# Performance work log

Hardware: AMD Instinct MI355X
Metric: run time of the kernel (lower is better)

The kernel has to match this reference:

```python
import jax, jax.numpy as jnp
import numpy as np

N, C, V, T = 256, 256, 25, 20
K = 3            # kernel_size
PAD = 1          # padding
O = 256          # out_channels
C4 = C // 4
EPS = 1e-5


def _bn(x, p, axes_shape):
    # p: (4, dim) = gamma, beta, running_mean, running_var (eval-mode BN)
    g, b, m, v = (p[i].reshape(axes_shape) for i in range(4))
    return (x - m) * (g / jnp.sqrt(v + EPS)) + b


def setup_inputs() -> dict:
    key = jax.random.key(0)
    ks = jax.random.split(key, 12)
    rn = lambda k, s, sc=0.05: jax.random.normal(k, s, jnp.float32) * sc
    bn = lambda k, d: jnp.stack([
        1.0 + 0.1 * jax.random.normal(jax.random.fold_in(k, 0), (d,), jnp.float32),  # gamma
        0.1 * jax.random.normal(jax.random.fold_in(k, 1), (d,), jnp.float32),        # beta
        0.1 * jax.random.normal(jax.random.fold_in(k, 2), (d,), jnp.float32),        # mean
        0.5 + jax.random.uniform(jax.random.fold_in(k, 3), (d,), jnp.float32),       # var
    ])
    return {
        "x": jax.random.normal(ks[0], (N, C, V, T), jnp.float32),
        "Wg1": rn(ks[1], (2 * T, T), 0.2),      # Linear T -> 2T (no bias)
        "Wg2": rn(ks[2], (K, 2 * T), 0.2),      # Linear 2T -> K (no bias)
        "Wl1": rn(ks[3], (C4, C, K)),           # Conv1d C -> C/4, kernel K
        "Wl2": rn(ks[4], (C, C4)),              # Conv1d C/4 -> C, kernel 1
        "Wc2": rn(ks[5], (O, C)),               # 1x1 Conv2d C -> O (no bias)
        "bng": bn(ks[6], 2 * T),
        "bnl": bn(ks[7], C4),
        "bn1p": bn(ks[8], C),
        "bn2p": bn(ks[9], O),
    }


def reference(x, Wg1, Wg2, Wl1, Wl2, Wc2, bng, bnl, bn1p, bn2p):
    n, c, v, t = x.shape
    new_x = jnp.transpose(x, (0, 1, 3, 2))            # (N, C, T, V)
    pooled = new_x.mean(axis=-1)                       # (N, C, T)  adaptive_avg_pool over V

    # --- G branch: per-(n,c) dynamic temporal kernel ---
    h = pooled.reshape(n * c, t) @ Wg1.T               # (NC, 2T)
    h = jax.nn.relu(_bn(h, bng, (1, 2 * t)))
    kern = jax.nn.softmax(h @ Wg2.T, axis=-1)          # (NC, K)
    kern = kern.reshape(n, c, K)

    # --- L branch: local temporal excitation ---
    l = jax.lax.conv_general_dilated(
        pooled, Wl1, window_strides=(1,), padding=[(K // 2, K // 2)],
        dimension_numbers=("NCH", "OIH", "NCH"))      # (N, C4, T)
    l = jax.nn.relu(_bn(l, bnl, (1, C4, 1)))
    l = jax.nn.sigmoid(jnp.einsum("oc,nct->not", Wl2, l))  # (N, C, T)
    new_x = new_x + l[..., None]                       # (N, C, T, V)

    # --- dynamic depthwise temporal conv (groups = N*C) ---
    padded = jnp.pad(new_x, ((0, 0), (0, 0), (PAD, PAD), (0, 0)))
    out = sum(kern[:, :, k, None, None] * padded[:, :, k:k + t, :] for k in range(K))

    out = jnp.transpose(out, (0, 1, 3, 2))             # (N, C, V, T)
    out = jax.nn.relu(_bn(out, bn1p, (1, c, 1, 1)))    # bn1 + relu; dropout in eval = identity
    out = jnp.einsum("oc,ncvt->novt", Wc2, out)        # 1x1 conv
    out = jax.nn.relu(_bn(out, bn2p, (1, O, 1, 1)))    # bn2 + relu
    return out
```

## Files before the change

### kernel.cpp

```cpp
#include <hip/hip_runtime.h>
#include <hip/hip_bf16.h>
#include <math.h>

#define N_ 256
#define C_ 256
#define V_ 25
#define T_ 20
#define C4_ 64
#define O_ 256
#define VT_ 500
#define EPS_ 1e-5f

typedef unsigned short ushort_t;
typedef unsigned short us4 __attribute__((ext_vector_type(4)));
typedef short short8 __attribute__((ext_vector_type(8)));
typedef float f32x4 __attribute__((ext_vector_type(4)));

__device__ __forceinline__ float bf2f(ushort_t u) {
    unsigned int v = ((unsigned int)u) << 16;
    return __builtin_bit_cast(float, v);
}
__device__ __forceinline__ ushort_t f2bf(float f) {
    unsigned int u = __builtin_bit_cast(unsigned int, f);
    unsigned int r = u + 0x7fffu + ((u >> 16) & 1u);
    return (ushort_t)(r >> 16);
}

__device__ __forceinline__ void bar_lds() {
    __builtin_amdgcn_sched_barrier(0);
    asm volatile("s_waitcnt lgkmcnt(0)" ::: "memory");
    __builtin_amdgcn_s_barrier();
    __builtin_amdgcn_sched_barrier(0);
}

__global__ __launch_bounds__(256) void k_pool(const float* __restrict__ x,
                                              float* __restrict__ pooled,
                                              const float* __restrict__ Wc2,
                                              ushort_t* __restrict__ wbf) {
    int tid = threadIdx.x;
    if (blockIdx.x >= 8192) {
        int i = (blockIdx.x - 8192) * 256 + tid;
        f32x4 v = ((const f32x4*)Wc2)[i];
        us4 o; o.x = f2bf(v.x); o.y = f2bf(v.y); o.z = f2bf(v.z); o.w = f2bf(v.w);
        ((us4*)wbf)[i] = o;
        return;
    }
    __shared__ float xs[8][504];
    const f32x4* src = (const f32x4*)(x + (size_t)blockIdx.x * 8 * VT_);
    for (int i = tid; i < 1000; i += 256) {
        int r = i / 125, cidx = (i % 125) * 4;
        *(f32x4*)&xs[r][cidx] = src[i];
    }
    __syncthreads();
    if (tid < 160) {
        int r = tid / 20, t = tid % 20;
        float s = 0.f;
#pragma unroll
        for (int v = 0; v < V_; ++v) s += xs[r][v * T_ + t];
        pooled[blockIdx.x * 160 + tid] = s * 0.04f;
    }
}

__global__ __launch_bounds__(256) void k_gl(const float* __restrict__ pooled,
                                            const float* __restrict__ Wg1,
                                            const float* __restrict__ Wg2,
                                            const float* __restrict__ Wl1,
                                            const float* __restrict__ Wl2,
                                            const float* __restrict__ bng,
                                            const float* __restrict__ bnl,
                                            float* __restrict__ kern,
                                            float* __restrict__ l2out) {
    __shared__ float pp[C_][22];
    __shared__ float wg1[800];
    __shared__ float wg2[120];
    __shared__ float sg[40], bg[40];
    __shared__ float ls[C4_][20];
    __shared__ float sl[C4_], bl[C4_];
    int tid = threadIdx.x;
    int n = blockIdx.x;

    for (int i = tid; i < 800; i += 256) wg1[i] = Wg1[i];
    if (tid < 120) wg2[tid] = Wg2[tid];
    if (tid < 40) {
        float g = bng[tid], b = bng[40 + tid];
        float m = bng[80 + tid], v = bng[120 + tid];
        float s = g * rsqrtf(v + EPS_);
        sg[tid] = s; bg[tid] = b - m * s;
    }
    if (tid < C4_) {
        float g = bnl[tid], b = bnl[64 + tid];
        float m = bnl[128 + tid], v = bnl[192 + tid];
        float s = g * rsqrtf(v + EPS_);
        sl[tid] = s; bl[tid] = b - m * s;
    }
    {
        const f32x4* pn = (const f32x4*)(pooled + n * (C_ * T_));
#pragma unroll
        for (int q = 0; q < 5; ++q) {
            int id = q * 256 + tid;
            int c = id / 5, qq = id % 5;
            f32x4 v = pn[id];
            pp[c][qq * 4 + 1] = v.x; pp[c][qq * 4 + 2] = v.y;
            pp[c][qq * 4 + 3] = v.z; pp[c][qq * 4 + 4] = v.w;
        }
        pp[tid][0] = 0.f; pp[tid][21] = 0.f;
    }
    __syncthreads();

    {
        int c = tid;
        float p[20];
#pragma unroll
        for (int t = 0; t < 20; ++t) p[t] = pp[c][t + 1];
        float l0 = 0.f, l1 = 0.f, l2 = 0.f;
#pragma unroll 4
        for (int j = 0; j < 40; ++j) {
            float h = 0.f;
#pragma unroll
            for (int t = 0; t < 20; ++t) h = fmaf(wg1[j * 20 + t], p[t], h);
            h = fmaxf(fmaf(h, sg[j], bg[j]), 0.f);
            l0 = fmaf(wg2[j], h, l0);
            l1 = fmaf(wg2[40 + j], h, l1);
            l2 = fmaf(wg2[80 + j], h, l2);
        }
        float mx = fmaxf(l0, fmaxf(l1, l2));
        float e0 = __expf(l0 - mx), e1 = __expf(l1 - mx), e2 = __expf(l2 - mx);
        float inv = 1.f / (e0 + e1 + e2);
        float* kp = kern + (n * C_ + c) * 3;
        kp[0] = e0 * inv; kp[1] = e1 * inv; kp[2] = e2 * inv;
    }

    {
        int c4 = tid >> 2;
        int t0 = (tid & 3) * 5;
        float acc0 = 0.f, acc1 = 0.f, acc2 = 0.f, acc3 = 0.f, acc4 = 0.f;
        const float* w = Wl1 + c4 * (C_ * 3);
#pragma unroll 8
        for (int c = 0; c < C_; ++c) {
            float w0 = w[c * 3 + 0];
            float w1 = w[c * 3 + 1];
            float w2 = w[c * 3 + 2];
            float a0 = pp[c][t0 + 0], a1 = pp[c][t0 + 1], a2 = pp[c][t0 + 2];
            float a3 = pp[c][t0 + 3], a4 = pp[c][t0 + 4], a5 = pp[c][t0 + 5];
            float a6 = pp[c][t0 + 6];
            acc0 = fmaf(w0, a0, fmaf(w1, a1, fmaf(w2, a2, acc0)));
            acc1 = fmaf(w0, a1, fmaf(w1, a2, fmaf(w2, a3, acc1)));
            acc2 = fmaf(w0, a2, fmaf(w1, a3, fmaf(w2, a4, acc2)));
            acc3 = fmaf(w0, a3, fmaf(w1, a4, fmaf(w2, a5, acc3)));
            acc4 = fmaf(w0, a4, fmaf(w1, a5, fmaf(w2, a6, acc4)));
        }
        float s = sl[c4], b = bl[c4];
        ls[c4][t0 + 0] = fmaxf(fmaf(acc0, s, b), 0.f);
        ls[c4][t0 + 1] = fmaxf(fmaf(acc1, s, b), 0.f);
        ls[c4][t0 + 2] = fmaxf(fmaf(acc2, s, b), 0.f);
        ls[c4][t0 + 3] = fmaxf(fmaf(acc3, s, b), 0.f);
        ls[c4][t0 + 4] = fmaxf(fmaf(acc4, s, b), 0.f);
    }
    __syncthreads();

    {
        int c = tid;
        float acc[20];
#pragma unroll
        for (int t = 0; t < 20; ++t) acc[t] = 0.f;
        const float* w = Wl2 + c * C4_;
#pragma unroll 4
        for (int c4 = 0; c4 < C4_; ++c4) {
            float wv = w[c4];
#pragma unroll
            for (int t = 0; t < 20; ++t) acc[t] = fmaf(wv, ls[c4][t], acc[t]);
        }
        f32x4* o = (f32x4*)(l2out + (n * C_ + c) * T_);
#pragma unroll
        for (int q = 0; q < 5; ++q) {
            f32x4 v;
            v.x = 1.f / (1.f + __expf(-acc[q*4+0]));
            v.y = 1.f / (1.f + __expf(-acc[q*4+1]));
            v.z = 1.f / (1.f + __expf(-acc[q*4+2]));
            v.w = 1.f / (1.f + __expf(-acc[q*4+3]));
            o[q] = v;
        }
    }
}

#define YSTRIDE 264

template <int NT>
__device__ __forceinline__ void gemm_pass(const ushort_t* __restrict__ yT,
                                          const ushort_t* __restrict__ wbf,
                                          float* __restrict__ outn,
                                          const int (&ctb)[NT], int ov_idx,
                                          int obase, int mrow, int kof, int prow,
                                          float s2, float b2) {
    f32x4 acc[4][NT];
#pragma unroll
    for (int mt = 0; mt < 4; ++mt)
#pragma unroll
        for (int j = 0; j < NT; ++j) acc[mt][j] = (f32x4){0.f, 0.f, 0.f, 0.f};

#pragma unroll 1
    for (int kk = 0; kk < C_; kk += 32) {
        short8 af[4];
        short8 bfr[NT];
#pragma unroll
        for (int mt = 0; mt < 4; ++mt)
            af[mt] = *(const short8*)(wbf + (obase + mt * 16 + mrow) * C_ + kk + kof);
#pragma unroll
        for (int j = 0; j < NT; ++j)
            bfr[j] = *(const short8*)(yT + (ctb[j] + mrow) * YSTRIDE + kk + kof);
#pragma unroll
        for (int mt = 0; mt < 4; ++mt)
#pragma unroll
            for (int j = 0; j < NT; ++j)
                acc[mt][j] = __builtin_amdgcn_mfma_f32_16x16x32_bf16(af[mt], bfr[j], acc[mt][j], 0, 0, 0);
    }

#pragma unroll
    for (int mt = 0; mt < 4; ++mt) {
#pragma unroll
        for (int r = 0; r < 4; ++r) {
            int lsrc = mt * 16 + prow + r;
            float s2w = __shfl(s2, lsrc);
            float b2w = __shfl(b2, lsrc);
            float* orow = outn + (size_t)(obase + lsrc) * VT_;
#pragma unroll
            for (int j = 0; j < NT; ++j) {
                bool skip = (j == ov_idx) && (mrow < 12);
                if (!skip) {
                    float vr = fmaxf(fmaf(acc[mt][j][r], s2w, b2w), 0.f);
                    orow[ctb[j] + mrow] = vr;
                }
            }
        }
    }
}

__global__ __launch_bounds__(256, 3) void k_main(const float* __restrict__ x,
                                                 const ushort_t* __restrict__ wbf,
                                                 const float* __restrict__ bn1p,
                                                 const float* __restrict__ bn2p,
                                                 const float* __restrict__ kern,
                                                 const float* __restrict__ l2g,
                                                 float* __restrict__ out) {
    __shared__ __align__(16) ushort_t yT[100 * YSTRIDE];

    int tid = threadIdx.x;
    int n = blockIdx.y;
    int vblk = blockIdx.x;
    const float* xn = x + (size_t)n * (C_ * V_ * T_) + vblk * 100;

    float s1, b1, k0, k1, k2, s2, b2, l2r[20];
    {
        int c = tid;
        float g1 = bn1p[c], be1 = bn1p[256 + c];
        float m1 = bn1p[512 + c], v1 = bn1p[768 + c];
        s1 = g1 * rsqrtf(v1 + EPS_);
        b1 = be1 - m1 * s1;
        float g2 = bn2p[c], be2 = bn2p[256 + c];
        float m2 = bn2p[512 + c], v2 = bn2p[768 + c];
        s2 = g2 * rsqrtf(v2 + EPS_);
        b2 = be2 - m2 * s2;
        const float* kp = kern + (n * C_ + c) * 3;
        k0 = kp[0]; k1 = kp[1]; k2 = kp[2];
        const f32x4* lp = (const f32x4*)(l2g + (n * C_ + c) * T_);
#pragma unroll
        for (int q = 0; q < 5; ++q) {
            f32x4 v = lp[q];
            l2r[q*4+0] = v.x; l2r[q*4+1] = v.y; l2r[q*4+2] = v.z; l2r[q*4+3] = v.w;
        }
    }

    int offg[5], offs[5];
#pragma unroll
    for (int q = 0; q < 5; ++q) {
        int id = q * 256 + tid;
        int c = id / 5, qq = id % 5;
        offg[q] = c * VT_ + qq * 4;
        offs[q] = c * 20 + qq * 4;
    }

    f32x4 ld[5];
#pragma unroll
    for (int q = 0; q < 5; ++q) ld[q] = *(const f32x4*)(xn + offg[q]);

    for (int vl = 0; vl < 5; ++vl) {
        f32x4 ldn[5];
        if (vl < 4) {
#pragma unroll
            for (int q = 0; q < 5; ++q)
                ldn[q] = *(const f32x4*)(xn + offg[q] + (vl + 1) * 20);
        }
        ushort_t* xs = yT + vl * 20 * YSTRIDE;
#pragma unroll
        for (int q = 0; q < 5; ++q) {
            us4 o; o.x = f2bf(ld[q].x); o.y = f2bf(ld[q].y);
            o.z = f2bf(ld[q].z); o.w = f2bf(ld[q].w);
            *(us4*)(xs + offs[q]) = o;
        }
        bar_lds();
        float a[22];
        a[0] = 0.f; a[21] = 0.f;
        {
            const ushort_t* xrow = xs + tid * 20;
#pragma unroll
            for (int qq = 0; qq < 5; ++qq) {
                us4 u = *(const us4*)(xrow + qq * 4);
                a[qq*4 + 1] = bf2f(u.x) + l2r[qq*4 + 0];
                a[qq*4 + 2] = bf2f(u.y) + l2r[qq*4 + 1];
                a[qq*4 + 3] = bf2f(u.z) + l2r[qq*4 + 2];
                a[qq*4 + 4] = bf2f(u.w) + l2r[qq*4 + 3];
            }
        }
        bar_lds();
        {
            ushort_t* yrow = yT + vl * 20 * YSTRIDE + tid;
#pragma unroll
            for (int t = 0; t < 20; ++t) {
                float z = fmaf(k0, a[t], fmaf(k1, a[t + 1], k2 * a[t + 2]));
                yrow[t * YSTRIDE] = f2bf(fmaxf(fmaf(z, s1, b1), 0.f));
            }
        }
        if (vl < 4) {
#pragma unroll
            for (int q = 0; q < 5; ++q) ld[q] = ldn[q];
        }
    }
    bar_lds();

    int lane = tid & 63;
    int wave = tid >> 6;
    int mrow = lane & 15;
    int kof = (lane >> 4) * 8;
    int prow = (lane >> 4) * 4;
    int obase = wave * 64;
    float* outn = out + (size_t)n * (O_ * VT_) + vblk * 100;

    {
        const int ctb0[4] = {0, 16, 32, 48};
        gemm_pass<4>(yT, wbf, outn, ctb0, -1, obase, mrow, kof, prow, s2, b2);
    }
    {
        const int ctb1[3] = {64, 80, 84};
        gemm_pass<3>(yT, wbf, outn, ctb1, 2, obase, mrow, kof, prow, s2, b2);
    }
}

extern "C" void kernel_launch(void* const* d_in, const int* in_sizes, int n_in,
                              void* d_out, int out_size, void* d_ws, size_t ws_size,
                              hipStream_t stream) {
    const float* x   = (const float*)d_in[0];
    const float* Wg1 = (const float*)d_in[1];
    const float* Wg2 = (const float*)d_in[2];
    const float* Wl1 = (const float*)d_in[3];
    const float* Wl2 = (const float*)d_in[4];
    const float* Wc2 = (const float*)d_in[5];
    const float* bng = (const float*)d_in[6];
    const float* bnl = (const float*)d_in[7];
    const float* bn1p = (const float*)d_in[8];
    const float* bn2p = (const float*)d_in[9];
    float* out = (float*)d_out;

    float* ws = (float*)d_ws;
    float* pooled = ws;
    float* kern   = ws + 1310720;
    float* l2g    = ws + 1310720 + 196608;
    ushort_t* wbf = (ushort_t*)(ws + 1310720 + 196608 + 1310720);

    k_pool<<<dim3(8256), dim3(256), 0, stream>>>(x, pooled, Wc2, wbf);
    k_gl<<<dim3(N_), dim3(256), 0, stream>>>(pooled, Wg1, Wg2, Wl1, Wl2, bng, bnl, kern, l2g);
    k_main<<<dim3(5, N_), dim3(256), 0, stream>>>(x, wbf, bn1p, bn2p, kern, l2g, out);
}
```

Measured before the change: 366.8 us.

## Move L-branch convolutions to bf16 MFMA and double-buffer x prefetch in main kernel

```diff
diff --git a/kernel.cpp b/kernel.cpp
--- a/kernel.cpp
+++ b/kernel.cpp
@@ -36,8 +36,27 @@
 __global__ __launch_bounds__(256) void k_pool(const float* __restrict__ x,
                                               float* __restrict__ pooled,
                                               const float* __restrict__ Wc2,
-                                              ushort_t* __restrict__ wbf) {
+                                              ushort_t* __restrict__ wbf,
+                                              const float* __restrict__ Wl1,
+                                              ushort_t* __restrict__ awl,
+                                              const float* __restrict__ Wl2,
+                                              ushort_t* __restrict__ wl2bf) {
     int tid = threadIdx.x;
+    if (blockIdx.x >= 8272) {
+        int o = (blockIdx.x - 8272) * 256 + tid;
+        int c4 = o / 768;
+        int rem = o - c4 * 768;
+        int k = rem >> 8, c = rem & 255;
+        awl[o] = f2bf(Wl1[(c4 * 256 + c) * 3 + k]);
+        return;
+    }
+    if (blockIdx.x >= 8256) {
+        int i = (blockIdx.x - 8256) * 256 + tid;
+        f32x4 v = ((const f32x4*)Wl2)[i];
+        us4 o; o.x = f2bf(v.x); o.y = f2bf(v.y); o.z = f2bf(v.z); o.w = f2bf(v.w);
+        ((us4*)wl2bf)[i] = o;
+        return;
+    }
     if (blockIdx.x >= 8192) {
         int i = (blockIdx.x - 8192) * 256 + tid;
         f32x4 v = ((const f32x4*)Wc2)[i];
@@ -64,28 +83,32 @@
 __global__ __launch_bounds__(256) void k_gl(const float* __restrict__ pooled,
                                             const float* __restrict__ Wg1,
                                             const float* __restrict__ Wg2,
-                                            const float* __restrict__ Wl1,
-                                            const float* __restrict__ Wl2,
                                             const float* __restrict__ bng,
                                             const float* __restrict__ bnl,
+                                            const ushort_t* __restrict__ awl,
+                                            const ushort_t* __restrict__ wl2bf,
                                             float* __restrict__ kern,
                                             float* __restrict__ l2out) {
-    __shared__ float pp[C_][22];
-    __shared__ float wg1[800];
-    __shared__ float wg2[120];
-    __shared__ float sg[40], bg[40];
-    __shared__ float ls[C4_][20];
-    __shared__ float sl[C4_], bl[C4_];
+    __shared__ __align__(16) char smem[76288];
+    float (*pp)[22] = (float (*)[22])smem;
+    float* sl = (float*)(smem + 22528);
+    float* bl = (float*)(smem + 22528 + 256);
+    char* lsT = smem + 23040;
+    char* bpt = smem + 27136;
+
     int tid = threadIdx.x;
     int n = blockIdx.x;
 
-    for (int i = tid; i < 800; i += 256) wg1[i] = Wg1[i];
-    if (tid < 120) wg2[tid] = Wg2[tid];
-    if (tid < 40) {
-        float g = bng[tid], b = bng[40 + tid];
-        float m = bng[80 + tid], v = bng[120 + tid];
-        float s = g * rsqrtf(v + EPS_);
-        sg[tid] = s; bg[tid] = b - m * s;
+    {
+        const f32x4* pn = (const f32x4*)(pooled + n * (C_ * T_));
+#pragma unroll
+        for (int q = 0; q < 5; ++q) {
+            int id = q * 256 + tid;
+            int c = id / 5, qq = id % 5;
+            f32x4 v = pn[id];
+            pp[c][qq * 4 + 0] = v.x; pp[c][qq * 4 + 1] = v.y;
+            pp[c][qq * 4 + 2] = v.z; pp[c][qq * 4 + 3] = v.w;
+        }
     }
     if (tid < C4_) {
         float g = bnl[tid], b = bnl[64 + tid];
@@ -94,91 +117,123 @@
         sl[tid] = s; bl[tid] = b - m * s;
     }
     {
-        const f32x4* pn = (const f32x4*)(pooled + n * (C_ * T_));
-#pragma unroll
-        for (int q = 0; q < 5; ++q) {
-            int id = q * 256 + tid;
-            int c = id / 5, qq = id % 5;
-            f32x4 v = pn[id];
-            pp[c][qq * 4 + 1] = v.x; pp[c][qq * 4 + 2] = v.y;
-            pp[c][qq * 4 + 3] = v.z; pp[c][qq * 4 + 4] = v.w;
-        }
-        pp[tid][0] = 0.f; pp[tid][21] = 0.f;
+        unsigned int* z = (unsigned int*)lsT;
+        for (int i = tid; i < 384; i += 256) z[640 + i] = 0u;
     }
     __syncthreads();
 
-    {
-        int c = tid;
-        float p[20];
-#pragma unroll
-        for (int t = 0; t < 20; ++t) p[t] = pp[c][t + 1];
+    float p[20];
+#pragma unroll
+    for (int t = 0; t < 20; ++t) p[t] = pp[tid][t];
+
+    {
         float l0 = 0.f, l1 = 0.f, l2 = 0.f;
 #pragma unroll 4
         for (int j = 0; j < 40; ++j) {
             float h = 0.f;
 #pragma unroll
-            for (int t = 0; t < 20; ++t) h = fmaf(wg1[j * 20 + t], p[t], h);
-            h = fmaxf(fmaf(h, sg[j], bg[j]), 0.f);
-            l0 = fmaf(wg2[j], h, l0);
-            l1 = fmaf(wg2[40 + j], h, l1);
-            l2 = fmaf(wg2[80 + j], h, l2);
+            for (int t = 0; t < 20; ++t) h = fmaf(Wg1[j * 20 + t], p[t], h);
+            float g = bng[j], b = bng[40 + j];
+            float m = bng[80 + j], v = bng[120 + j];
+            float s = g * rsqrtf(v + EPS_);
+            h = fmaxf(fmaf(h, s, b - m * s), 0.f);
+            l0 = fmaf(Wg2[j], h, l0);
+            l1 = fmaf(Wg2[40 + j], h, l1);
+            l2 = fmaf(Wg2[80 + j], h, l2);
         }
         float mx = fmaxf(l0, fmaxf(l1, l2));
         float e0 = __expf(l0 - mx), e1 = __expf(l1 - mx), e2 = __expf(l2 - mx);
         float inv = 1.f / (e0 + e1 + e2);
-        float* kp = kern + (n * C_ + c) * 3;
+        float* kp = kern + (n * C_ + tid) * 3;
         kp[0] = e0 * inv; kp[1] = e1 * inv; kp[2] = e2 * inv;
     }
 
     {
-        int c4 = tid >> 2;
-        int t0 = (tid & 3) * 5;
-        float acc0 = 0.f, acc1 = 0.f, acc2 = 0.f, acc3 = 0.f, acc4 = 0.f;
-        const float* w = Wl1 + c4 * (C_ * 3);
-#pragma unroll 8
-        for (int c = 0; c < C_; ++c) {
-            float w0 = w[c * 3 + 0];
-            float w1 = w[c * 3 + 1];
-            float w2 = w[c * 3 + 2];
-            float a0 = pp[c][t0 + 0], a1 = pp[c][t0 + 1], a2 = pp[c][t0 + 2];
-            float a3 = pp[c][t0 + 3], a4 = pp[c][t0 + 4], a5 = pp[c][t0 + 5];
-            float a6 = pp[c][t0 + 6];
-            acc0 = fmaf(w0, a0, fmaf(w1, a1, fmaf(w2, a2, acc0)));
-            acc1 = fmaf(w0, a1, fmaf(w1, a2, fmaf(w2, a3, acc1)));
-            acc2 = fmaf(w0, a2, fmaf(w1, a3, fmaf(w2, a4, acc2)));
-            acc3 = fmaf(w0, a3, fmaf(w1, a4, fmaf(w2, a5, acc3)));
-            acc4 = fmaf(w0, a4, fmaf(w1, a5, fmaf(w2, a6, acc4)));
-        }
-        float s = sl[c4], b = bl[c4];
-        ls[c4][t0 + 0] = fmaxf(fmaf(acc0, s, b), 0.f);
-        ls[c4][t0 + 1] = fmaxf(fmaf(acc1, s, b), 0.f);
-        ls[c4][t0 + 2] = fmaxf(fmaf(acc2, s, b), 0.f);
-        ls[c4][t0 + 3] = fmaxf(fmaf(acc3, s, b), 0.f);
-        ls[c4][t0 + 4] = fmaxf(fmaf(acc4, s, b), 0.f);
+        int c = tid;
+#pragma unroll
+        for (int k = 0; k < 3; ++k) {
+            int col2base = (k * 256 + c) * 2;
+#pragma unroll
+            for (int t = 0; t < 20; ++t) {
+                int i = t + k - 1;
+                float v = (i >= 0 && i < 20) ? p[i] : 0.f;
+                int byte = t * 1536 + (col2base ^ ((t & 7) << 4));
+                *(ushort_t*)(bpt + byte) = f2bf(v);
+            }
+        }
     }
     __syncthreads();
 
-    {
-        int c = tid;
-        float acc[20];
-#pragma unroll
-        for (int t = 0; t < 20; ++t) acc[t] = 0.f;
-        const float* w = Wl2 + c * C4_;
+    int lane = tid & 63, wave = tid >> 6;
+    int mrow = lane & 15, kof = (lane >> 4) * 8, prow = (lane >> 4) * 4;
+
+    {
+        f32x4 acc0 = (f32x4){0.f, 0.f, 0.f, 0.f};
+        f32x4 acc1 = (f32x4){0.f, 0.f, 0.f, 0.f};
+        int swz = ((mrow & 7) << 4);
 #pragma unroll 4
-        for (int c4 = 0; c4 < C4_; ++c4) {
-            float wv = w[c4];
-#pragma unroll
-            for (int t = 0; t < 20; ++t) acc[t] = fmaf(wv, ls[c4][t], acc[t]);
-        }
-        f32x4* o = (f32x4*)(l2out + (n * C_ + c) * T_);
-#pragma unroll
-        for (int q = 0; q < 5; ++q) {
-            f32x4 v;
-            v.x = 1.f / (1.f + __expf(-acc[q*4+0]));
-            v.y = 1.f / (1.f + __expf(-acc[q*4+1]));
-            v.z = 1.f / (1.f + __expf(-acc[q*4+2]));
-            v.w = 1.f / (1.f + __expf(-acc[q*4+3]));
-            o[q] = v;
+        for (int kk = 0; kk < 768; kk += 32) {
+            short8 af = *(const short8*)(awl + (wave * 16 + mrow) * 768 + kk + kof);
+            short8 b0 = *(const short8*)(bpt + mrow * 1536 + (((kk + kof) * 2) ^ swz));
+            short8 b1 = *(const short8*)(bpt + (16 + mrow) * 1536 + (((kk + kof) * 2) ^ swz));
+            acc0 = __builtin_amdgcn_mfma_f32_16x16x32_bf16(af, b0, acc0, 0, 0, 0);
+            acc1 = __builtin_amdgcn_mfma_f32_16x16x32_bf16(af, b1, acc1, 0, 0, 0);
+        }
+        f32x4 sv = *(const f32x4*)(sl + wave * 16 + prow);
+        f32x4 bv = *(const f32x4*)(bl + wave * 16 + prow);
+#pragma unroll
+        for (int nt = 0; nt < 2; ++nt) {
+            int t = nt * 16 + (lane & 15);
+            if (t < 20) {
+                f32x4 a = nt ? acc1 : acc0;
+#pragma unroll
+                for (int r = 0; r < 4; ++r) {
+                    int c4 = wave * 16 + prow + r;
+                    float v = fmaxf(fmaf(a[r], sv[r], bv[r]), 0.f);
+                    int byte = t * 128 + ((c4 * 2) ^ ((t & 7) << 4));
+                    *(ushort_t*)(lsT + byte) = f2bf(v);
+                }
+            }
+        }
+    }
+    __syncthreads();
+
+    {
+        f32x4 acc[4][2];
+#pragma unroll
+        for (int mtl = 0; mtl < 4; ++mtl)
+#pragma unroll
+            for (int nt = 0; nt < 2; ++nt) acc[mtl][nt] = (f32x4){0.f, 0.f, 0.f, 0.f};
+        int swz = ((mrow & 7) << 4);
+#pragma unroll
+        for (int kk = 0; kk < 64; kk += 32) {
+            short8 af[4], bfr[2];
+#pragma unroll
+            for (int mtl = 0; mtl < 4; ++mtl)
+                af[mtl] = *(const short8*)(wl2bf + (wave * 64 + mtl * 16 + mrow) * 64 + kk + kof);
+#pragma unroll
+            for (int nt = 0; nt < 2; ++nt)
+                bfr[nt] = *(const short8*)(lsT + (nt * 16 + mrow) * 128 + (((kk + kof) * 2) ^ swz));
+#pragma unroll
+            for (int mtl = 0; mtl < 4; ++mtl)
+#pragma unroll
+                for (int nt = 0; nt < 2; ++nt)
+                    acc[mtl][nt] = __builtin_amdgcn_mfma_f32_16x16x32_bf16(af[mtl], bfr[nt], acc[mtl][nt], 0, 0, 0);
+        }
+#pragma unroll
+        for (int nt = 0; nt < 2; ++nt) {
+            int t = nt * 16 + (lane & 15);
+            if (t < 20) {
+#pragma unroll
+                for (int mtl = 0; mtl < 4; ++mtl) {
+#pragma unroll
+                    for (int r = 0; r < 4; ++r) {
+                        int c = wave * 64 + mtl * 16 + prow + r;
+                        float v = acc[mtl][nt][r];
+                        l2out[(n * C_ + c) * T_ + t] = 1.f / (1.f + __expf(-v));
+                    }
+                }
+            }
         }
     }
 }
@@ -279,23 +334,26 @@
         offs[q] = c * 20 + qq * 4;
     }
 
-    f32x4 ld[5];
-#pragma unroll
-    for (int q = 0; q < 5; ++q) ld[q] = *(const f32x4*)(xn + offg[q]);
-
+    f32x4 ld[2][5];
+#pragma unroll
+    for (int q = 0; q < 5; ++q) ld[0][q] = *(const f32x4*)(xn + offg[q]);
+#pragma unroll
+    for (int q = 0; q < 5; ++q) ld[1][q] = *(const f32x4*)(xn + offg[q] + 20);
+
+#pragma unroll
     for (int vl = 0; vl < 5; ++vl) {
-        f32x4 ldn[5];
-        if (vl < 4) {
+        const int cur = vl & 1;
+        ushort_t* xs = yT + vl * 20 * YSTRIDE;
+#pragma unroll
+        for (int q = 0; q < 5; ++q) {
+            us4 o; o.x = f2bf(ld[cur][q].x); o.y = f2bf(ld[cur][q].y);
+            o.z = f2bf(ld[cur][q].z); o.w = f2bf(ld[cur][q].w);
+            *(us4*)(xs + offs[q]) = o;
+        }
+        if (vl < 3) {
 #pragma unroll
             for (int q = 0; q < 5; ++q)
-                ldn[q] = *(const f32x4*)(xn + offg[q] + (vl + 1) * 20);
-        }
-        ushort_t* xs = yT + vl * 20 * YSTRIDE;
-#pragma unroll
-        for (int q = 0; q < 5; ++q) {
-            us4 o; o.x = f2bf(ld[q].x); o.y = f2bf(ld[q].y);
-            o.z = f2bf(ld[q].z); o.w = f2bf(ld[q].w);
-            *(us4*)(xs + offs[q]) = o;
+                ld[cur][q] = *(const f32x4*)(xn + offg[q] + (vl + 2) * 20);
         }
         bar_lds();
         float a[22];
@@ -319,10 +377,6 @@
                 float z = fmaf(k0, a[t], fmaf(k1, a[t + 1], k2 * a[t + 2]));
                 yrow[t * YSTRIDE] = f2bf(fmaxf(fmaf(z, s1, b1), 0.f));
             }
-        }
-        if (vl < 4) {
-#pragma unroll
-            for (int q = 0; q < 5; ++q) ld[q] = ldn[q];
         }
     }
     bar_lds();
@@ -364,9 +418,11 @@
     float* pooled = ws;
     float* kern   = ws + 1310720;
     float* l2g    = ws + 1310720 + 196608;
-    ushort_t* wbf = (ushort_t*)(ws + 1310720 + 196608 + 1310720);
-
-    k_pool<<<dim3(8256), dim3(256), 0, stream>>>(x, pooled, Wc2, wbf);
-    k_gl<<<dim3(N_), dim3(256), 0, stream>>>(pooled, Wg1, Wg2, Wl1, Wl2, bng, bnl, kern, l2g);
+    ushort_t* wbf   = (ushort_t*)(ws + 2818048);
+    ushort_t* wl2bf = (ushort_t*)(ws + 2818048 + 32768);
+    ushort_t* awl   = (ushort_t*)(ws + 2818048 + 40960);
+
+    k_pool<<<dim3(8464), dim3(256), 0, stream>>>(x, pooled, Wc2, wbf, Wl1, awl, Wl2, wl2bf);
+    k_gl<<<dim3(N_), dim3(256), 0, stream>>>(pooled, Wg1, Wg2, bng, bnl, awl, wl2bf, kern, l2g);
     k_main<<<dim3(5, N_), dim3(256), 0, stream>>>(x, wbf, bn1p, bn2p, kern, l2g, out);
 }
```

Result: faster. 352.5 us (-3.9%).
